# Optimization experiments

Measured on AMD Instinct MI355X. Metric: run time of the kernel, lower is better.

The kernel has to match this reference:

```python
import jax, jax.numpy as jnp
import numpy as np


def _conv1x1_relu(x, W, b):
    # x: (B, Cin, N, k), W: (Cout, Cin), b: (Cout,) -> (B, Cout, N, k)
    return jax.nn.relu(jnp.einsum('bcnk,oc->bonk', x, W) + b[None, :, None, None])


def _knn_idx(pc, k):
    # pc: (B, C, N). Mirrors torch: dis_mat = -||pi - pj||^2, topk (largest) -> nearest.
    G = jnp.einsum('bcn,bcm->bnm', pc, pc)            # (B, N, N)
    sq = jnp.sum(pc * pc, axis=1)                      # (B, N)
    neg_dist = 2.0 * G - sq[:, :, None] - sq[:, None, :]
    _, idx = jax.lax.top_k(neg_dist, k)                # (B, N, k) int32
    return idx


def _group_points(x, idx):
    # x: (B, C, N), idx: (B, N, k) -> (B, C, N, k); out[b,c,n,j] = x[b,c,idx[b,n,j]]
    B, C, N = x.shape
    k = idx.shape[-1]
    idx2 = jnp.broadcast_to(idx.reshape(B, 1, N * k), (B, C, N * k))
    return jnp.take_along_axis(x, idx2, axis=2).reshape(B, C, N, k)


def setup_inputs() -> dict:
    key = jax.random.key(0)
    ks = jax.random.split(key, 8)
    B, N, C, O, K = 8, 4096, 64, 64, 16
    s = 0.05
    return {
        'xyz': jax.random.normal(ks[0], (B, 3, N), dtype=jnp.float32),
        'fea': jax.random.normal(ks[1], (B, C, N), dtype=jnp.float32),
        'Wg1': jax.random.normal(ks[2], (O, 10), dtype=jnp.float32) * s,
        'bg1': jnp.zeros((O,), dtype=jnp.float32),
        'Wg2': jax.random.normal(ks[3], (O, O), dtype=jnp.float32) * s,
        'bg2': jnp.zeros((O,), dtype=jnp.float32),
        'Wf1': jax.random.normal(ks[4], (O, 2 * C), dtype=jnp.float32) * s,
        'bf1': jnp.zeros((O,), dtype=jnp.float32),
        'Wf2': jax.random.normal(ks[5], (O, O), dtype=jnp.float32) * s,
        'bf2': jnp.zeros((O,), dtype=jnp.float32),
        'Wf3': jax.random.normal(ks[6], (O, O), dtype=jnp.float32) * s,
        'bf3': jnp.zeros((O,), dtype=jnp.float32),
        'k': 16,
    }


def reference(xyz, fea, Wg1, bg1, Wg2, bg2, Wf1, bf1, Wf2, bf2, Wf3, bf3, k):
    idx = _knn_idx(fea, k)                             # (B, N, k)

    # get_edge_point: (B, 10, N, k)
    xyz_knn = _group_points(xyz, idx)                  # (B, 3, N, k)
    xyz_c = jnp.broadcast_to(xyz[:, :, :, None], xyz_knn.shape)
    xyz_r = xyz_c - xyz_knn
    xyz_d = jnp.sqrt(jnp.sum(xyz_r * xyz_r, axis=1, keepdims=True))
    geo = jnp.concatenate([xyz_d, xyz_c, xyz_knn, xyz_r], axis=1)

    # get_edge_feature: (B, 2C, N, k)
    fea_knn = _group_points(fea, idx)
    fea_c = jnp.broadcast_to(fea[:, :, :, None], fea_knn.shape)
    edge = jnp.concatenate([fea_c, fea_knn], axis=1)

    g = _conv1x1_relu(geo, Wg1, bg1)
    g = _conv1x1_relu(g, Wg2, bg2)

    f = _conv1x1_relu(edge, Wf1, bf1)
    f = _conv1x1_relu(f, Wf2, bf2)
    f = _conv1x1_relu(f, Wf3, bf3)

    out = jnp.max(g * f, axis=-1)                      # (B, O, N)
    return out
```

## Files before the change

kernel.cpp:

```cpp
#include <hip/hip_runtime.h>
#include <math.h>

#define NB 8
#define NPTS 4096
#define NCH 64
#define NOUT 64
#define KNN 16

#define GLOBAL_AS const __attribute__((address_space(1)))
#define LDS_AS __attribute__((address_space(3)))

#define WS_SQ  0
#define WS_PT  (NB*NPTS)
#define WS_QT  (WS_PT + NB*NPTS*64)
#define WS_IDX (WS_QT + NB*NPTS*64)

__global__ __launch_bounds__(256) void k_sq(const float* __restrict__ fea,
                                            float* __restrict__ sq) {
    int g = blockIdx.x * 256 + threadIdx.x;
    int b = g >> 12, n = g & 4095;
    const float* f = fea + (size_t)b * NCH * NPTS + n;
    float s = 0.f;
#pragma unroll
    for (int c = 0; c < NCH; ++c) s = fmaf(f[c * NPTS], f[c * NPTS], s);
    sq[g] = s;
}

__global__ __launch_bounds__(256, 4) void k_knn(const float* __restrict__ fea,
                                                const float* __restrict__ sq,
                                                int* __restrict__ idxout) {
    __shared__ __align__(16) float rowT[64][32];
    __shared__ __align__(16) float colT[2][64 * 64];

    const int b = blockIdx.y;
    const int n0 = blockIdx.x * 32;
    const int tid = threadIdx.x;
    const int lane = tid & 63, w = tid >> 6;
    const int g = lane >> 4, p = lane & 15;
    const int rbase = w * 8 + g * 2;
    const float* feab = fea + (size_t)b * NCH * NPTS;

    auto stage = [&](int buf, int m0) {
#pragma unroll
        for (int i = 0; i < 4; ++i) {
            int k = w * 4 + i;
            int c = 4 * k + (lane >> 4);
            int j = (lane & 15) * 4;
            const float* gp = feab + c * NPTS + m0 + j;
            float* lp = &colT[buf][k * 256];
            __builtin_amdgcn_global_load_lds((GLOBAL_AS void*)gp,
                                             (LDS_AS void*)lp, 16, 0, 0);
        }
    };

#pragma unroll
    for (int i = 0; i < 2; ++i) {
        int e = i * 1024 + tid * 4;
        int c = e >> 5, r = e & 31;
        *(float4*)&rowT[c][r] = *(const float4*)&feab[c * NPTS + n0 + r];
    }

    float lstv[2];
    int   lsti[2];
    float thr[2];
#pragma unroll
    for (int i = 0; i < 2; ++i) {
        lstv[i] = -3.0e38f; lsti[i] = 0; thr[i] = -3.0e38f;
    }

    auto ins = [&](int i, float vv, int col) {
        unsigned long long lt = __ballot(lstv[i] < vv);
        int pos = __popc((unsigned)((lt >> (g * 16)) & 0xFFFFu));
        int nv = __builtin_amdgcn_update_dpp(0, __float_as_int(lstv[i]),
                                             0x101, 0xF, 0xF, true);
        int ni = __builtin_amdgcn_update_dpp(0, lsti[i],
                                             0x101, 0xF, 0xF, true);
        if (p <= pos - 2)      { lstv[i] = __int_as_float(nv); lsti[i] = ni; }
        else if (p == pos - 1) { lstv[i] = vv; lsti[i] = col; }
    };

    stage(0, 0);
    __syncthreads();

    for (int t = 0; t < 64; ++t) {
        const int m0 = t * 64;
        const int cur = t & 1;
        if (t < 63) stage(cur ^ 1, m0 + 64);

        float4 sqc = *(const float4*)&sq[b * NPTS + m0 + p * 4];

        float acc[2][4] = {{0.f,0.f,0.f,0.f},{0.f,0.f,0.f,0.f}};
#pragma unroll 8
        for (int c = 0; c < 64; ++c) {
            float2 rv = *(const float2*)&rowT[c][rbase];
            float4 cv = *(const float4*)&colT[cur][c * 64 + p * 4];
            float cc[4] = {cv.x, cv.y, cv.z, cv.w};
#pragma unroll
            for (int ci = 0; ci < 4; ++ci) {
                acc[0][ci] = fmaf(rv.x, cc[ci], acc[0][ci]);
                acc[1][ci] = fmaf(rv.y, cc[ci], acc[1][ci]);
            }
        }

        float sqa[4] = {sqc.x, sqc.y, sqc.z, sqc.w};
#pragma unroll
        for (int i = 0; i < 2; ++i)
#pragma unroll
            for (int j = 0; j < 4; ++j)
                acc[i][j] = fmaf(2.f, acc[i][j], -sqa[j]);

#pragma unroll
        for (int i = 0; i < 2; ++i) {
            float v0 = acc[i][0], v1 = acc[i][1];
            float v2 = acc[i][2], v3 = acc[i][3];
            float vm = fmaxf(fmaxf(v0, v1), fmaxf(v2, v3));
            unsigned long long bal = __ballot(vm > thr[i]);
            unsigned mg = (unsigned)((bal >> (g * 16)) & 0xFFFFull);
            while (__any(mg != 0u)) {
                bool act = (mg != 0u);
                int srcp = act ? (__ffs(mg) - 1) : 0;
                mg &= (mg - 1u);
                int srcl = (g << 4) | srcp;
                float b0 = __shfl(v0, srcl);
                float b1 = __shfl(v1, srcl);
                float b2 = __shfl(v2, srcl);
                float b3 = __shfl(v3, srcl);
                if (act) {
                    int cb = m0 + srcp * 4;
                    if (b0 > thr[i]) ins(i, b0, cb + 0);
                    if (b1 > thr[i]) ins(i, b1, cb + 1);
                    if (b2 > thr[i]) ins(i, b2, cb + 2);
                    if (b3 > thr[i]) ins(i, b3, cb + 3);
                }
            }
            if (bal) thr[i] = __shfl(lstv[i], 0, 16);
        }
        __syncthreads();
    }

#pragma unroll
    for (int i = 0; i < 2; ++i) {
        int row = rbase + i;
        idxout[((size_t)(b * NPTS) + n0 + row) * KNN + (15 - p)] = lsti[i];
    }
}

__global__ __launch_bounds__(256) void k_pq(const float* __restrict__ fea,
                                            const float* __restrict__ Wf1,
                                            const float* __restrict__ bf1,
                                            float* __restrict__ Pt,
                                            float* __restrict__ Qt) {
    __shared__ __align__(16) float feaT[64][64];
    __shared__ __align__(16) float WT[64][132];
    __shared__ float sb[64];

    const int b = blockIdx.y;
    const int n0 = blockIdx.x * 64;
    const int tid = threadIdx.x;
    const int to = tid & 15, tn = tid >> 4;
    const float* feab = fea + (size_t)b * NCH * NPTS;

#pragma unroll
    for (int i = 0; i < 4; ++i) {
        int e = i * 1024 + tid * 4;
        int c = e >> 6, nn = e & 63;
        *(float4*)&feaT[c][nn] = *(const float4*)&feab[c * NPTS + n0 + nn];
    }
#pragma unroll
    for (int i = 0; i < 8; ++i) {
        int g = tid * 32 + i * 4;
        int op = g >> 6, c = g & 63;
        const float* src = (op < 64) ? &Wf1[op * 128 + c]
                                     : &Wf1[(op - 64) * 128 + 64 + c];
        float4 w = *(const float4*)src;
        WT[c + 0][op] = w.x; WT[c + 1][op] = w.y;
        WT[c + 2][op] = w.z; WT[c + 3][op] = w.w;
    }
    if (tid < 64) sb[tid] = bf1[tid];
    __syncthreads();

    float acc[4][8];
#pragma unroll
    for (int ni = 0; ni < 4; ++ni)
#pragma unroll
        for (int oj = 0; oj < 8; ++oj) acc[ni][oj] = 0.f;

#pragma unroll 4
    for (int c = 0; c < 64; ++c) {
        float4 a  = *(const float4*)&feaT[c][tn * 4];
        float4 w0 = *(const float4*)&WT[c][to * 8];
        float4 w1 = *(const float4*)&WT[c][to * 8 + 4];
        float av[4] = {a.x, a.y, a.z, a.w};
        float wv[8] = {w0.x, w0.y, w0.z, w0.w, w1.x, w1.y, w1.z, w1.w};
#pragma unroll
        for (int ni = 0; ni < 4; ++ni)
#pragma unroll
            for (int oj = 0; oj < 8; ++oj)
                acc[ni][oj] = fmaf(av[ni], wv[oj], acc[ni][oj]);
    }

    const int opb = to * 8;
#pragma unroll
    for (int ni = 0; ni < 4; ++ni) {
        int n = n0 + tn * 4 + ni;
        size_t base = ((size_t)b * NPTS + n) * 64;
        if (opb < 64) {
            float4 o0, o1;
            o0.x = acc[ni][0] + sb[opb + 0]; o0.y = acc[ni][1] + sb[opb + 1];
            o0.z = acc[ni][2] + sb[opb + 2]; o0.w = acc[ni][3] + sb[opb + 3];
            o1.x = acc[ni][4] + sb[opb + 4]; o1.y = acc[ni][5] + sb[opb + 5];
            o1.z = acc[ni][6] + sb[opb + 6]; o1.w = acc[ni][7] + sb[opb + 7];
            *(float4*)&Pt[base + opb]     = o0;
            *(float4*)&Pt[base + opb + 4] = o1;
        } else {
            float4 o0, o1;
            o0.x = acc[ni][0]; o0.y = acc[ni][1]; o0.z = acc[ni][2]; o0.w = acc[ni][3];
            o1.x = acc[ni][4]; o1.y = acc[ni][5]; o1.z = acc[ni][6]; o1.w = acc[ni][7];
            *(float4*)&Qt[base + opb - 64]     = o0;
            *(float4*)&Qt[base + opb - 64 + 4] = o1;
        }
    }
}

__global__ __launch_bounds__(256) void k_mlp(
    const float* __restrict__ xyz,
    const float* __restrict__ Pt, const float* __restrict__ Qt,
    const int* __restrict__ knnidx,
    const float* __restrict__ Wg1, const float* __restrict__ bg1,
    const float* __restrict__ Wg2, const float* __restrict__ bg2,
    const float* __restrict__ Wf2, const float* __restrict__ bf2,
    const float* __restrict__ Wf3, const float* __restrict__ bf3,
    float* __restrict__ out) {
    __shared__ __align__(16) float bufX[64][68];
    __shared__ __align__(16) float bufY[64][68];
    __shared__ __align__(16) float WbufA[64][68];
    __shared__ __align__(16) float WbufB[64][68];
    __shared__ __align__(16) float scratch[1280];
    __shared__ float biasA[64], biasB[64];
    __shared__ int sidx[64];

    const int b = blockIdx.y;
    const int n0 = blockIdx.x * 4;
    const int tid = threadIdx.x;
    const int to = tid & 15, tp = tid >> 4;

    if (tid < 64)
        sidx[tid] = knnidx[((size_t)(b * NPTS + n0)) * KNN + tid];
    __syncthreads();

    {
        int pair = tid >> 2, q = tid & 3;
        int m = sidx[pair];
        int pt = pair >> 4;
        const float* pB = &Pt[((size_t)b * NPTS + n0 + pt) * 64];
        const float* qB = &Qt[((size_t)b * NPTS + m) * 64];
#pragma unroll
        for (int i = 0; i < 4; ++i) {
            int c0 = q * 16 + i * 4;
            float4 pv = *(const float4*)&pB[c0];
            float4 qv = *(const float4*)&qB[c0];
            bufX[c0 + 0][pair] = fmaxf(pv.x + qv.x, 0.f);
            bufX[c0 + 1][pair] = fmaxf(pv.y + qv.y, 0.f);
            bufX[c0 + 2][pair] = fmaxf(pv.z + qv.z, 0.f);
            bufX[c0 + 3][pair] = fmaxf(pv.w + qv.w, 0.f);
        }
    }
    if (tid < 64) {
        int pair = tid, pt = pair >> 4;
        int m = sidx[pair];
        const float* xb = xyz + (size_t)b * 3 * NPTS;
        float cx = xb[0 * NPTS + n0 + pt], cy = xb[1 * NPTS + n0 + pt], cz = xb[2 * NPTS + n0 + pt];
        float kx = xb[0 * NPTS + m], ky = xb[1 * NPTS + m], kz = xb[2 * NPTS + m];
        float rx = cx - kx, ry = cy - ky, rz = cz - kz;
        float d = sqrtf(rx * rx + ry * ry + rz * rz);
        scratch[0 * 68 + pair] = d;
        scratch[1 * 68 + pair] = cx; scratch[2 * 68 + pair] = cy; scratch[3 * 68 + pair] = cz;
        scratch[4 * 68 + pair] = kx; scratch[5 * 68 + pair] = ky; scratch[6 * 68 + pair] = kz;
        scratch[7 * 68 + pair] = rx; scratch[8 * 68 + pair] = ry; scratch[9 * 68 + pair] = rz;
    }

    auto stageW = [&](const float* W, const float* bv, float (*Wb)[68],
                      float* bias) {
#pragma unroll
        for (int i = 0; i < 4; ++i) {
            int g = tid * 16 + i * 4;
            int o = g >> 6, c = g & 63;
            float4 w = *(const float4*)&W[g];
            Wb[c + 0][o] = w.x; Wb[c + 1][o] = w.y;
            Wb[c + 2][o] = w.z; Wb[c + 3][o] = w.w;
        }
        if (tid < 64) bias[tid] = bv[tid];
    };

    auto gemmPh = [&](const float* src, float* dst, int Kdim,
                      const float (*Wb)[68], const float* bias) {
        float acc[4][4] = {{0.f,0.f,0.f,0.f},{0.f,0.f,0.f,0.f},
                           {0.f,0.f,0.f,0.f},{0.f,0.f,0.f,0.f}};
#pragma unroll 2
        for (int c = 0; c < Kdim; ++c) {
            float4 w = *(const float4*)&Wb[c][tp * 4];
            float4 a = *(const float4*)(src + c * 68 + to * 4);
            float wr[4] = {w.x, w.y, w.z, w.w};
            float ar[4] = {a.x, a.y, a.z, a.w};
#pragma unroll
            for (int oi = 0; oi < 4; ++oi)
#pragma unroll
                for (int pj = 0; pj < 4; ++pj)
                    acc[oi][pj] = fmaf(wr[oi], ar[pj], acc[oi][pj]);
        }
#pragma unroll
        for (int oi = 0; oi < 4; ++oi) {
            float bo = bias[tp * 4 + oi];
            float4 o4;
            o4.x = fmaxf(acc[oi][0] + bo, 0.f);
            o4.y = fmaxf(acc[oi][1] + bo, 0.f);
            o4.z = fmaxf(acc[oi][2] + bo, 0.f);
            o4.w = fmaxf(acc[oi][3] + bo, 0.f);
            *(float4*)(dst + (tp * 4 + oi) * 68 + to * 4) = o4;
        }
    };

    stageW(Wf2, bf2, WbufA, biasA);
    stageW(Wf3, bf3, WbufB, biasB);
    __syncthreads();
    gemmPh(&bufX[0][0], &bufY[0][0], 64, WbufA, biasA);
    __syncthreads();
    gemmPh(&bufY[0][0], &bufX[0][0], 64, WbufB, biasB);
    {
        for (int e = tid; e < 640; e += 256) {
            int o = e / 10, c = e - o * 10;
            WbufA[c][o] = Wg1[e];
        }
        if (tid < 64) biasA[tid] = bg1[tid];
    }
    __syncthreads();
    gemmPh(scratch, &bufY[0][0], 10, WbufA, biasA);
    stageW(Wg2, bg2, WbufB, biasB);
    __syncthreads();
    {
        float acc[4][4] = {{0.f,0.f,0.f,0.f},{0.f,0.f,0.f,0.f},
                           {0.f,0.f,0.f,0.f},{0.f,0.f,0.f,0.f}};
#pragma unroll 2
        for (int c = 0; c < 64; ++c) {
            float4 w = *(const float4*)&WbufB[c][tp * 4];
            float4 a = *(const float4*)&bufY[c][to * 4];
            float wr[4] = {w.x, w.y, w.z, w.w};
            float ar[4] = {a.x, a.y, a.z, a.w};
#pragma unroll
            for (int oi = 0; oi < 4; ++oi)
#pragma unroll
                for (int pj = 0; pj < 4; ++pj)
                    acc[oi][pj] = fmaf(wr[oi], ar[pj], acc[oi][pj]);
        }
#pragma unroll
        for (int oi = 0; oi < 4; ++oi) {
            int o = tp * 4 + oi;
            float bo = biasB[o];
            float4 f3q = *(const float4*)&bufX[o][to * 4];
            float m0_ = fmaxf(acc[oi][0] + bo, 0.f) * f3q.x;
            float m1_ = fmaxf(acc[oi][1] + bo, 0.f) * f3q.y;
            float m2_ = fmaxf(acc[oi][2] + bo, 0.f) * f3q.z;
            float m3_ = fmaxf(acc[oi][3] + bo, 0.f) * f3q.w;
            scratch[o * 17 + to] =
                fmaxf(fmaxf(m0_, m1_), fmaxf(m2_, m3_));
        }
    }
    __syncthreads();
    {
        int o = tid & 63, pt = tid >> 6;
        float m0_ = scratch[o * 17 + pt * 4 + 0];
        float m1  = scratch[o * 17 + pt * 4 + 1];
        float m2  = scratch[o * 17 + pt * 4 + 2];
        float m3  = scratch[o * 17 + pt * 4 + 3];
        out[((size_t)b * 64 + o) * NPTS + n0 + pt] =
            fmaxf(fmaxf(m0_, m1), fmaxf(m2, m3));
    }
}

extern "C" void kernel_launch(void* const* d_in, const int* in_sizes, int n_in,
                              void* d_out, int out_size, void* d_ws, size_t ws_size,
                              hipStream_t stream) {
    const float* xyz = (const float*)d_in[0];
    const float* fea = (const float*)d_in[1];
    const float* Wg1 = (const float*)d_in[2];
    const float* bg1 = (const float*)d_in[3];
    const float* Wg2 = (const float*)d_in[4];
    const float* bg2 = (const float*)d_in[5];
    const float* Wf1 = (const float*)d_in[6];
    const float* bf1 = (const float*)d_in[7];
    const float* Wf2 = (const float*)d_in[8];
    const float* bf2 = (const float*)d_in[9];
    const float* Wf3 = (const float*)d_in[10];
    const float* bf3 = (const float*)d_in[11];
    float* out = (float*)d_out;
    float* ws = (float*)d_ws;

    float* sq = ws + WS_SQ;
    float* Pt = ws + WS_PT;
    float* Qt = ws + WS_QT;
    int* idxw = (int*)(ws + WS_IDX);

    k_sq  <<<dim3(128),      dim3(256), 0, stream>>>(fea, sq);
    k_knn <<<dim3(128, 8),   dim3(256), 0, stream>>>(fea, sq, idxw);
    k_pq  <<<dim3(64, 8),    dim3(256), 0, stream>>>(fea, Wf1, bf1, Pt, Qt);
    k_mlp <<<dim3(1024, 8),  dim3(256), 0, stream>>>(xyz, Pt, Qt, idxw,
                                                     Wg1, bg1, Wg2, bg2,
                                                     Wf2, bf2, Wf3, bf3, out);
}
```

Baseline: 646.1 us.

## Fuse squared-norm into PQ kernel and keep f3 in registers for max reduction

Removes the separate k_sq launch by computing per-point squared norms inside k_pq from the already staged LDS tile, and launches k_pq before k_knn. In k_mlp, the third feature-layer result is kept in registers instead of being written back to LDS. The final max over k neighbours uses warp shuffles instead of a scratch round trip and an extra barrier. This cuts one kernel launch, one global pass over fea and some LDS traffic and syncs, at the cost of higher register pressure in k_mlp.

```diff
diff --git a/kernel.cpp b/kernel.cpp
--- a/kernel.cpp
+++ b/kernel.cpp
@@ -14,17 +14,6 @@
 #define WS_PT  (NB*NPTS)
 #define WS_QT  (WS_PT + NB*NPTS*64)
 #define WS_IDX (WS_QT + NB*NPTS*64)
-
-__global__ __launch_bounds__(256) void k_sq(const float* __restrict__ fea,
-                                            float* __restrict__ sq) {
-    int g = blockIdx.x * 256 + threadIdx.x;
-    int b = g >> 12, n = g & 4095;
-    const float* f = fea + (size_t)b * NCH * NPTS + n;
-    float s = 0.f;
-#pragma unroll
-    for (int c = 0; c < NCH; ++c) s = fmaf(f[c * NPTS], f[c * NPTS], s);
-    sq[g] = s;
-}
 
 __global__ __launch_bounds__(256, 4) void k_knn(const float* __restrict__ fea,
                                                 const float* __restrict__ sq,
@@ -149,7 +138,8 @@
                                             const float* __restrict__ Wf1,
                                             const float* __restrict__ bf1,
                                             float* __restrict__ Pt,
-                                            float* __restrict__ Qt) {
+                                            float* __restrict__ Qt,
+                                            float* __restrict__ sq) {
     __shared__ __align__(16) float feaT[64][64];
     __shared__ __align__(16) float WT[64][132];
     __shared__ float sb[64];
@@ -178,6 +168,16 @@
     }
     if (tid < 64) sb[tid] = bf1[tid];
     __syncthreads();
+
+    if (tid < 64) {
+        float s = 0.f;
+#pragma unroll
+        for (int c = 0; c < 64; ++c) {
+            float v = feaT[c][tid];
+            s = fmaf(v, v, s);
+        }
+        sq[b * NPTS + n0 + tid] = s;
+    }
 
     float acc[4][8];
 #pragma unroll
@@ -235,7 +235,7 @@
     __shared__ __align__(16) float bufY[64][68];
     __shared__ __align__(16) float WbufA[64][68];
     __shared__ __align__(16) float WbufB[64][68];
-    __shared__ __align__(16) float scratch[1280];
+    __shared__ __align__(16) float geoS[10 * 68];
     __shared__ float biasA[64], biasB[64];
     __shared__ int sidx[64];
 
@@ -273,10 +273,10 @@
         float kx = xb[0 * NPTS + m], ky = xb[1 * NPTS + m], kz = xb[2 * NPTS + m];
         float rx = cx - kx, ry = cy - ky, rz = cz - kz;
         float d = sqrtf(rx * rx + ry * ry + rz * rz);
-        scratch[0 * 68 + pair] = d;
-        scratch[1 * 68 + pair] = cx; scratch[2 * 68 + pair] = cy; scratch[3 * 68 + pair] = cz;
-        scratch[4 * 68 + pair] = kx; scratch[5 * 68 + pair] = ky; scratch[6 * 68 + pair] = kz;
-        scratch[7 * 68 + pair] = rx; scratch[8 * 68 + pair] = ry; scratch[9 * 68 + pair] = rz;
+        geoS[0 * 68 + pair] = d;
+        geoS[1 * 68 + pair] = cx; geoS[2 * 68 + pair] = cy; geoS[3 * 68 + pair] = cz;
+        geoS[4 * 68 + pair] = kx; geoS[5 * 68 + pair] = ky; geoS[6 * 68 + pair] = kz;
+        geoS[7 * 68 + pair] = rx; geoS[8 * 68 + pair] = ry; geoS[9 * 68 + pair] = rz;
     }
 
     auto stageW = [&](const float* W, const float* bv, float (*Wb)[68],
@@ -323,20 +323,11 @@
     stageW(Wf2, bf2, WbufA, biasA);
     stageW(Wf3, bf3, WbufB, biasB);
     __syncthreads();
+
     gemmPh(&bufX[0][0], &bufY[0][0], 64, WbufA, biasA);
     __syncthreads();
-    gemmPh(&bufY[0][0], &bufX[0][0], 64, WbufB, biasB);
-    {
-        for (int e = tid; e < 640; e += 256) {
-            int o = e / 10, c = e - o * 10;
-            WbufA[c][o] = Wg1[e];
-        }
-        if (tid < 64) biasA[tid] = bg1[tid];
-    }
-    __syncthreads();
-    gemmPh(scratch, &bufY[0][0], 10, WbufA, biasA);
-    stageW(Wg2, bg2, WbufB, biasB);
-    __syncthreads();
+
+    float f3r[4][4];
     {
         float acc[4][4] = {{0.f,0.f,0.f,0.f},{0.f,0.f,0.f,0.f},
                            {0.f,0.f,0.f,0.f},{0.f,0.f,0.f,0.f}};
@@ -354,26 +345,64 @@
         }
 #pragma unroll
         for (int oi = 0; oi < 4; ++oi) {
-            int o = tp * 4 + oi;
-            float bo = biasB[o];
-            float4 f3q = *(const float4*)&bufX[o][to * 4];
-            float m0_ = fmaxf(acc[oi][0] + bo, 0.f) * f3q.x;
-            float m1_ = fmaxf(acc[oi][1] + bo, 0.f) * f3q.y;
-            float m2_ = fmaxf(acc[oi][2] + bo, 0.f) * f3q.z;
-            float m3_ = fmaxf(acc[oi][3] + bo, 0.f) * f3q.w;
-            scratch[o * 17 + to] =
-                fmaxf(fmaxf(m0_, m1_), fmaxf(m2_, m3_));
-        }
-    }
-    __syncthreads();
+            float bo = biasB[tp * 4 + oi];
+            f3r[oi][0] = fmaxf(acc[oi][0] + bo, 0.f);
+            f3r[oi][1] = fmaxf(acc[oi][1] + bo, 0.f);
+            f3r[oi][2] = fmaxf(acc[oi][2] + bo, 0.f);
+            f3r[oi][3] = fmaxf(acc[oi][3] + bo, 0.f);
+        }
+    }
     {
-        int o = tid & 63, pt = tid >> 6;
-        float m0_ = scratch[o * 17 + pt * 4 + 0];
-        float m1  = scratch[o * 17 + pt * 4 + 1];
-        float m2  = scratch[o * 17 + pt * 4 + 2];
-        float m3  = scratch[o * 17 + pt * 4 + 3];
-        out[((size_t)b * 64 + o) * NPTS + n0 + pt] =
-            fmaxf(fmaxf(m0_, m1), fmaxf(m2, m3));
+        for (int e = tid; e < 640; e += 256) {
+            int o = e / 10, c = e - o * 10;
+            WbufA[c][o] = Wg1[e];
+        }
+        if (tid < 64) biasA[tid] = bg1[tid];
+    }
+    __syncthreads();
+
+    gemmPh(geoS, &bufY[0][0], 10, WbufA, biasA);
+    stageW(Wg2, bg2, WbufB, biasB);
+    __syncthreads();
+
+    {
+        float acc[4][4] = {{0.f,0.f,0.f,0.f},{0.f,0.f,0.f,0.f},
+                           {0.f,0.f,0.f,0.f},{0.f,0.f,0.f,0.f}};
+#pragma unroll 2
+        for (int c = 0; c < 64; ++c) {
+            float4 w = *(const float4*)&WbufB[c][tp * 4];
+            float4 a = *(const float4*)&bufY[c][to * 4];
+            float wr[4] = {w.x, w.y, w.z, w.w};
+            float ar[4] = {a.x, a.y, a.z, a.w};
+#pragma unroll
+            for (int oi = 0; oi < 4; ++oi)
+#pragma unroll
+                for (int pj = 0; pj < 4; ++pj)
+                    acc[oi][pj] = fmaf(wr[oi], ar[pj], acc[oi][pj]);
+        }
+        float mx[4];
+#pragma unroll
+        for (int oi = 0; oi < 4; ++oi) {
+            float bo = biasB[tp * 4 + oi];
+            float m0_ = fmaxf(acc[oi][0] + bo, 0.f) * f3r[oi][0];
+            float m1_ = fmaxf(acc[oi][1] + bo, 0.f) * f3r[oi][1];
+            float m2_ = fmaxf(acc[oi][2] + bo, 0.f) * f3r[oi][2];
+            float m3_ = fmaxf(acc[oi][3] + bo, 0.f) * f3r[oi][3];
+            mx[oi] = fmaxf(fmaxf(m0_, m1_), fmaxf(m2_, m3_));
+        }
+#pragma unroll
+        for (int oi = 0; oi < 4; ++oi) {
+            mx[oi] = fmaxf(mx[oi], __shfl_xor(mx[oi], 1));
+            mx[oi] = fmaxf(mx[oi], __shfl_xor(mx[oi], 2));
+        }
+        if ((to & 3) == 0) {
+            int pt = to >> 2;
+#pragma unroll
+            for (int oi = 0; oi < 4; ++oi) {
+                int o = tp * 4 + oi;
+                out[((size_t)b * 64 + o) * NPTS + n0 + pt] = mx[oi];
+            }
+        }
     }
 }
 
@@ -400,9 +429,8 @@
     float* Qt = ws + WS_QT;
     int* idxw = (int*)(ws + WS_IDX);
 
-    k_sq  <<<dim3(128),      dim3(256), 0, stream>>>(fea, sq);
+    k_pq  <<<dim3(64, 8),    dim3(256), 0, stream>>>(fea, Wf1, bf1, Pt, Qt, sq);
     k_knn <<<dim3(128, 8),   dim3(256), 0, stream>>>(fea, sq, idxw);
-    k_pq  <<<dim3(64, 8),    dim3(256), 0, stream>>>(fea, Wf1, bf1, Pt, Qt);
     k_mlp <<<dim3(1024, 8),  dim3(256), 0, stream>>>(xyz, Pt, Qt, idxw,
                                                      Wg1, bg1, Wg2, bg2,
                                                      Wf2, bf2, Wf3, bf3, out);
```

Result: faster. 622.3 us, median of 2 (-3.7%).
